# Optimization experiments

Hardware: AMD Instinct MI355X
Metric: run time of the kernel (lower is better)

## Reference

```python
import jax, jax.numpy as jnp
import numpy as np

IN_F, RED, WID, CLS, T = 700, 256, 4096, 20, 100


def _q4(W):
    # per-tensor symmetric INT4 STE: value is quantized, grad is identity
    scale = jnp.maximum(jnp.abs(W).max() / 7.0, 1e-8)
    return W + jax.lax.stop_gradient(jnp.round(W / scale) * scale - W)


def setup_inputs() -> dict:
    key = jax.random.key(0)
    ks = jax.random.split(key, 12)
    B = 64
    x = jax.random.normal(ks[0], (B, T, IN_F), dtype=jnp.float32)
    latent = jax.random.uniform(ks[1], (T,), dtype=jnp.float32)
    spatial_W = jax.random.normal(ks[2], (RED, IN_F), jnp.float32) / np.sqrt(IN_F)
    spatial_b = jnp.zeros((RED,), jnp.float32)
    conv_W = jax.random.normal(ks[3], (RED, RED, 5), jnp.float32) / np.sqrt(RED * 5)
    conv_b = jnp.zeros((RED,), jnp.float32)
    fc1_W = jax.random.normal(ks[4], (WID, RED), jnp.float32) / np.sqrt(RED)
    fc1_b = jnp.zeros((WID,), jnp.float32)
    fc2_W = jax.random.normal(ks[5], (CLS, WID), jnp.float32) / np.sqrt(WID)
    fc2_b = jnp.zeros((CLS,), jnp.float32)
    gain = jnp.asarray(1.0, jnp.float32)
    return {"x": x, "latent": latent, "spatial_W": spatial_W, "spatial_b": spatial_b,
            "conv_W": conv_W, "conv_b": conv_b, "fc1_W": fc1_W, "fc1_b": fc1_b,
            "fc2_W": fc2_W, "fc2_b": fc2_b, "gain": gain}


def _compute_drive(x, latent, spatial_W, spatial_b, conv_W, conv_b, fc1_W, fc1_b, gain):
    # spatial projection (INT4 STE linear) + relu : (B,T,RED)
    xp = jax.nn.relu(jnp.einsum("btf,rf->btr", x, _q4(spatial_W)) + spatial_b)
    # temporal conv1d over T, padding=2 (same), channels RED->RED
    xc = jax.lax.conv_general_dilated(
        xp.transpose(0, 2, 1), conv_W, window_strides=(1,), padding=[(2, 2)],
        dimension_numbers=("NCH", "OIH", "NCH"))
    conv_out = jax.nn.relu(xc + conv_b[None, :, None]).transpose(0, 2, 1)  # (B,T,RED)
    spatial_act = jax.nn.softplus(jnp.einsum("btr,wr->btw", conv_out, _q4(fc1_W)) + fc1_b)
    return spatial_act * latent[None, :, None] * jnp.abs(gain)  # (B,T,WID)


def reference(x, latent, spatial_W, spatial_b, conv_W, conv_b, fc1_W, fc1_b, fc2_W, fc2_b, gain):
    drive = _compute_drive(x, latent, spatial_W, spatial_b, conv_W, conv_b, fc1_W, fc1_b, gain)
    # Poisson spike sampling with straight-through estimator, then clamp at 1
    pois = jax.random.poisson(jax.random.key(42), jax.lax.stop_gradient(drive)).astype(drive.dtype)
    spikes = drive + jax.lax.stop_gradient(pois - drive)
    spikes = jnp.minimum(spikes, 1.0)
    # decay-weighted temporal reduction over T
    decay = jnp.exp(jnp.linspace(-2.0, 0.0, T)).astype(drive.dtype)
    weighted = jnp.einsum("btw,t->bw", spikes, decay)  # (B,WID)
    # dropout in eval mode = identity
    logits = weighted @ _q4(fc2_W).T + fc2_b  # (B,CLS)
    return (logits, spikes, drive)
```

## Files before the change

kernel.cpp:

```cpp
#include <hip/hip_runtime.h>
#include <stdint.h>

#define B 64
#define T 100
#define IN_F 700
#define RED 256
#define WID 4096
#define CLS 20
#define BT (B*T)
#define NELEM (BT*WID)
#define LOGITS_OFF 0
#define SPIKES_OFF (B*CLS)
#define DRIVE_OFF (SPIKES_OFF + NELEM)

#define WS_SLOTS 0
#define WS_W2Q 16
#define WS_XP  (WS_W2Q + CLS*WID)
#define WS_CO  (WS_XP + BT*RED)
#define WS_WEIGHTED (WS_CO + BT*RED)

#define SC_WST 0
#define SC_W1T (SC_WST + IN_F*RED)
#define SC_CWT (SC_W1T + RED*WID)

__host__ __device__ __forceinline__ uint32_t rotl32(uint32_t v, int r) {
  return (v << r) | (v >> (32 - r));
}

__host__ __device__ __forceinline__ void threefry2x32(uint32_t k0, uint32_t k1,
                                                      uint32_t x0, uint32_t x1,
                                                      uint32_t& o0, uint32_t& o1) {
  uint32_t k2 = k0 ^ k1 ^ 0x1BD11BDAu;
  x0 += k0; x1 += k1;
#define TF_R(r) { x0 += x1; x1 = rotl32(x1, (r)); x1 ^= x0; }
  TF_R(13) TF_R(15) TF_R(26) TF_R(6)
  x0 += k1; x1 += k2 + 1u;
  TF_R(17) TF_R(29) TF_R(16) TF_R(24)
  x0 += k2; x1 += k0 + 2u;
  TF_R(13) TF_R(15) TF_R(26) TF_R(6)
  x0 += k0; x1 += k1 + 3u;
  TF_R(17) TF_R(29) TF_R(16) TF_R(24)
  x0 += k1; x1 += k2 + 4u;
  TF_R(13) TF_R(15) TF_R(26) TF_R(6)
  x0 += k2; x1 += k0 + 5u;
#undef TF_R
  o0 = x0; o1 = x1;
}

__global__ void absmax_kernel(const float* __restrict__ w, int n, uint32_t* slot) {
  __shared__ uint32_t sm[256];
  uint32_t m = 0u;
  for (int i = blockIdx.x * 256 + threadIdx.x; i < n; i += gridDim.x * 256)
    m = max(m, __float_as_uint(fabsf(w[i])));
  sm[threadIdx.x] = m;
  __syncthreads();
  for (int s = 128; s > 0; s >>= 1) {
    if (threadIdx.x < s) sm[threadIdx.x] = max(sm[threadIdx.x], sm[threadIdx.x + s]);
    __syncthreads();
  }
  if (threadIdx.x == 0) atomicMax(slot, sm[0]);
}

__global__ void quant_t_kernel(const float* __restrict__ w, float* __restrict__ qT,
                               int Nn, int Kk, const uint32_t* __restrict__ slot) {
  float s = fmaxf(__uint_as_float(*slot) / 7.0f, 1e-8f);
  int id = blockIdx.x * 256 + threadIdx.x;
  if (id < Nn * Kk) {
    int n = id / Kk, k = id - n * Kk;
    qT[(size_t)k * Nn + n] = rintf(w[id] / s) * s;
  }
}

__global__ void quant_kernel(const float* __restrict__ w, float* __restrict__ q,
                             int n, const uint32_t* __restrict__ slot) {
  float s = fmaxf(__uint_as_float(*slot) / 7.0f, 1e-8f);
  int i = blockIdx.x * 256 + threadIdx.x;
  if (i < n) q[i] = rintf(w[i] / s) * s;
}

__global__ void convw_t_kernel(const float* __restrict__ w, float* __restrict__ wt) {
  int id = blockIdx.x * 256 + threadIdx.x;
  if (id < 256 * 1280) {
    int o = id / 1280, r = id - o * 1280;
    int ic = r / 5, h = r - ic * 5;
    wt[(size_t)((h << 8) + ic) * 256 + o] = w[id];
  }
}

template<int SRCA>
__global__ __launch_bounds__(256, 8)
void gemm32_kernel(const float* __restrict__ A, const float* __restrict__ Bt,
                   const float* __restrict__ bias, float* __restrict__ C,
                   int M, int N, int K) {
  constexpr int MT = 32, NT = 64, TM = 2, TN = 4;
  constexpr int ASR = MT + 4, BSR = NT + 4;
  __shared__ float As[32 * ASR];
  __shared__ float Bs[32 * BSR];
  int tid = threadIdx.x;
  int tx = tid & 15, ty = tid >> 4;
  int m0 = blockIdx.x * MT, n0 = blockIdx.y * NT;
  float acc[TM * TN];
#pragma unroll
  for (int i = 0; i < TM * TN; ++i) acc[i] = 0.f;

  for (int kt = 0; kt < K; kt += 32) {
    int klen = K - kt; if (klen > 32) klen = 32;
#pragma unroll
    for (int rep = 0; rep < 4; ++rep) {
      int e = rep * 256 + tid;
      int kk = e & 31, m = e >> 5;
      float v = 0.f;
      if (SRCA == 0) {
        if (kk < klen) v = A[(size_t)(m0 + m) * K + kt + kk];
      } else {
        if (kk < klen) {
          int k = kt + kk;
          int h = k >> 8, ic = k & 255;
          int bt = m0 + m;
          int b = bt / T, t = bt - b * T;
          int tt = t + h - 2;
          if (tt >= 0 && tt < T) v = A[((size_t)(b * T + tt)) * RED + ic];
        }
      }
      As[kk * ASR + m] = v;
    }
#pragma unroll
    for (int rep = 0; rep < 8; ++rep) {
      int e = rep * 256 + tid;
      int kk = e >> 6, n = e & 63;
      float v = 0.f;
      if (kk < klen) v = Bt[(size_t)(kt + kk) * N + n0 + n];
      Bs[kk * BSR + n] = v;
    }
    __syncthreads();
    if (klen == 32) {
#pragma unroll
      for (int kk = 0; kk < 32; ++kk) {
        float a[TM], b[TN];
#pragma unroll
        for (int i = 0; i < TM; ++i) a[i] = As[kk * ASR + ty * TM + i];
#pragma unroll
        for (int d = 0; d < TN; ++d) b[d] = Bs[kk * BSR + tx * TN + d];
#pragma unroll
        for (int j = 0; j < TM; ++j)
#pragma unroll
          for (int d = 0; d < TN; ++d)
            acc[j * TN + d] = fmaf(a[j], b[d], acc[j * TN + d]);
      }
    } else {
      for (int kk = 0; kk < klen; ++kk) {
        float a[TM], b[TN];
#pragma unroll
        for (int i = 0; i < TM; ++i) a[i] = As[kk * ASR + ty * TM + i];
#pragma unroll
        for (int d = 0; d < TN; ++d) b[d] = Bs[kk * BSR + tx * TN + d];
#pragma unroll
        for (int j = 0; j < TM; ++j)
#pragma unroll
          for (int d = 0; d < TN; ++d)
            acc[j * TN + d] = fmaf(a[j], b[d], acc[j * TN + d]);
      }
    }
    __syncthreads();
  }

  float bv[TN];
#pragma unroll
  for (int d = 0; d < TN; ++d) bv[d] = bias[n0 + tx * TN + d];
#pragma unroll
  for (int j = 0; j < TM; ++j) {
    int m = m0 + ty * TM + j;
#pragma unroll
    for (int d = 0; d < TN; ++d)
      C[(size_t)m * N + n0 + tx * TN + d] = fmaxf(acc[j * TN + d] + bv[d], 0.0f);
  }
}

__global__ __launch_bounds__(256, 4)
void fc1_kernel(const float* __restrict__ A, const float* __restrict__ Bt,
                const float* __restrict__ bias, const float* __restrict__ latent,
                const float* __restrict__ gain, float* __restrict__ C,
                int K, int N) {
  constexpr int MT = 128, NT = 128, TM = 8, TN = 8;
  constexpr int ASR = MT + 4, BSR = NT + 4;
  __shared__ float As[32 * ASR];
  __shared__ float Bs[32 * BSR];
  int tid = threadIdx.x;
  int tx = tid & 15, ty = tid >> 4;
  int wid = (blockIdx.x & 7) * 200 + (blockIdx.x >> 3);
  int bx = wid % 50, by = wid / 50;
  int m0 = bx * MT, n0 = by * NT;
  float acc[TM * TN];
#pragma unroll
  for (int i = 0; i < TM * TN; ++i) acc[i] = 0.f;

  for (int kt = 0; kt < K; kt += 32) {
#pragma unroll
    for (int rep = 0; rep < 4; ++rep) {
      int e = rep * 256 + tid;
      int k4 = e & 7, m = e >> 3;
      const float4 v = *(const float4*)&A[(size_t)(m0 + m) * K + kt + k4 * 4];
      As[(k4 * 4 + 0) * ASR + m] = v.x;
      As[(k4 * 4 + 1) * ASR + m] = v.y;
      As[(k4 * 4 + 2) * ASR + m] = v.z;
      As[(k4 * 4 + 3) * ASR + m] = v.w;
    }
#pragma unroll
    for (int rep = 0; rep < 4; ++rep) {
      int e = rep * 256 + tid;
      int n4 = e & 31, kk = e >> 5;
      float4 v = *(const float4*)&Bt[(size_t)(kt + kk) * N + n0 + n4 * 4];
      *(float4*)&Bs[kk * BSR + n4 * 4] = v;
    }
    __syncthreads();
#pragma unroll
    for (int kk = 0; kk < 32; ++kk) {
      float a[TM], b[TN];
#pragma unroll
      for (int i = 0; i < TM; ++i) a[i] = As[kk * ASR + ty * TM + i];
#pragma unroll
      for (int d = 0; d < TN; ++d) b[d] = Bs[kk * BSR + tx * TN + d];
#pragma unroll
      for (int j = 0; j < TM; ++j)
#pragma unroll
        for (int d = 0; d < TN; ++d)
          acc[j * TN + d] = fmaf(a[j], b[d], acc[j * TN + d]);
    }
    __syncthreads();
  }

  float g = fabsf(gain[0]);
  float bv[TN];
#pragma unroll
  for (int d = 0; d < TN; ++d) bv[d] = bias[n0 + tx * TN + d];
#pragma unroll
  for (int j = 0; j < TM; ++j) {
    int bt = m0 + ty * TM + j;
    int q = bt / T;
    float lat = latent[bt - q * T];
    float o[TN];
#pragma unroll
    for (int d = 0; d < TN; ++d) {
      float v = acc[j * TN + d] + bv[d];
      float e = expf(-fabsf(v));
      float l = log1pf(e);
      float sp = fmaxf(v, 0.0f) + l;
      o[d] = (sp * lat) * g;
    }
    float4 o0 = make_float4(o[0], o[1], o[2], o[3]);
    float4 o1 = make_float4(o[4], o[5], o[6], o[7]);
    *(float4*)&C[(size_t)bt * N + n0 + tx * TN + 0] = o0;
    *(float4*)&C[(size_t)bt * N + n0 + tx * TN + 4] = o1;
  }
}

__global__ __launch_bounds__(256) void spike_weighted_kernel(float* __restrict__ out,
                                                             float* __restrict__ wt,
                                                             uint32_t k0, uint32_t k1) {
  __shared__ float dec[128];
  int tid = threadIdx.x;
  if (tid < T) {
    float step = 2.0f / 99.0f;
    float a = step * (float)tid;
    dec[tid] = expf(a - 2.0f);
  }
  __syncthreads();
  int b = blockIdx.x >> 4;
  int w = ((blockIdx.x & 15) << 8) + tid;
  float acc = 0.f;
  for (int t = 0; t < T; ++t) {
    uint32_t p = (uint32_t)((b * T + t) * WID + w);
    float lam = out[DRIVE_OFF + p];
    uint32_t y0, y1;
    threefry2x32(k0, k1, 0u, p, y0, y1);
    uint32_t bits = y0 ^ y1;
    float u = __uint_as_float((bits >> 9) | 0x3f800000u) - 1.0f;
    float s = (lam > 0.0f && logf(u) > -lam) ? 1.0f : 0.0f;
    out[SPIKES_OFF + p] = s;
    acc = fmaf(s, dec[t], acc);
  }
  wt[b * WID + w] = acc;
}

__global__ void logits_kernel(const float* __restrict__ wt,
                              const float* __restrict__ w2,
                              const float* __restrict__ b2,
                              float* __restrict__ out) {
  __shared__ float sm[256];
  int b = blockIdx.x / CLS, c = blockIdx.x - b * CLS;
  const float* wr = wt + (size_t)b * WID;
  const float* w2r = w2 + (size_t)c * WID;
  float p = 0.f;
  for (int w = threadIdx.x; w < WID; w += 256) p = fmaf(wr[w], w2r[w], p);
  sm[threadIdx.x] = p;
  __syncthreads();
  for (int s = 128; s > 0; s >>= 1) {
    if (threadIdx.x < s) sm[threadIdx.x] += sm[threadIdx.x + s];
    __syncthreads();
  }
  if (threadIdx.x == 0) out[LOGITS_OFF + blockIdx.x] = sm[0] + b2[c];
}

extern "C" void kernel_launch(void* const* d_in, const int* in_sizes, int n_in,
                              void* d_out, int out_size, void* d_ws, size_t ws_size,
                              hipStream_t stream) {
  (void)in_sizes; (void)n_in; (void)out_size; (void)ws_size;
  const float* x         = (const float*)d_in[0];
  const float* latent    = (const float*)d_in[1];
  const float* spatial_W = (const float*)d_in[2];
  const float* spatial_b = (const float*)d_in[3];
  const float* conv_W    = (const float*)d_in[4];
  const float* conv_b    = (const float*)d_in[5];
  const float* fc1_W     = (const float*)d_in[6];
  const float* fc1_b     = (const float*)d_in[7];
  const float* fc2_W     = (const float*)d_in[8];
  const float* fc2_b     = (const float*)d_in[9];
  const float* gain      = (const float*)d_in[10];
  float* out = (float*)d_out;
  uint32_t* wsu = (uint32_t*)d_ws;
  float* wsf = (float*)d_ws;
  float* S = out + SPIKES_OFF;

  uint32_t sk0, sk1;
  threefry2x32(0u, 42u, 0u, 1u, sk0, sk1);

  hipMemsetAsync(wsu + WS_SLOTS, 0, 3 * sizeof(uint32_t), stream);
  absmax_kernel<<<64, 256, 0, stream>>>(spatial_W, RED * IN_F, wsu + WS_SLOTS + 0);
  absmax_kernel<<<256, 256, 0, stream>>>(fc1_W, WID * RED, wsu + WS_SLOTS + 1);
  absmax_kernel<<<32, 256, 0, stream>>>(fc2_W, CLS * WID, wsu + WS_SLOTS + 2);

  quant_t_kernel<<<700, 256, 0, stream>>>(spatial_W, S + SC_WST, RED, IN_F, wsu + WS_SLOTS + 0);
  quant_t_kernel<<<4096, 256, 0, stream>>>(fc1_W, S + SC_W1T, WID, RED, wsu + WS_SLOTS + 1);
  quant_kernel<<<320, 256, 0, stream>>>(fc2_W, wsf + WS_W2Q, CLS * WID, wsu + WS_SLOTS + 2);
  convw_t_kernel<<<1280, 256, 0, stream>>>(conv_W, S + SC_CWT);

  gemm32_kernel<0><<<dim3(200, 4), 256, 0, stream>>>(
      x, S + SC_WST, spatial_b, wsf + WS_XP, BT, RED, IN_F);

  gemm32_kernel<1><<<dim3(200, 4), 256, 0, stream>>>(
      wsf + WS_XP, S + SC_CWT, conv_b, wsf + WS_CO, BT, RED, 1280);

  fc1_kernel<<<1600, 256, 0, stream>>>(
      wsf + WS_CO, S + SC_W1T, fc1_b, latent, gain, out + DRIVE_OFF, RED, WID);

  spike_weighted_kernel<<<B * 16, 256, 0, stream>>>(out, wsf + WS_WEIGHTED, sk0, sk1);

  logits_kernel<<<B * CLS, 256, 0, stream>>>(wsf + WS_WEIGHTED, wsf + WS_W2Q, fc2_b, out);
}
```

Measured before the change: 843.1 us.

## Fuse fc1 weight quantization into fc1 GEMM and vectorize gemm32 tile loads

Drops the separate quant_t kernel for fc1_W. The fc1 GEMM now reads the raw row-major weight, quantizes it on the fly using the absmax slot, and writes it transposed into shared memory. The fc1 thread-to-column mapping changes to two 4-wide halves to suit the new Bs layout. The gemm32 A and B tile loads become float4 loads with fewer iterations. The fused path repeats the division and rounding in every block that touches a weight tile, and its transposed shared-memory stores may cause bank conflicts.

After: 734.8 us. 1.15x faster.

```diff
diff --git a/kernel.cpp b/kernel.cpp
--- a/kernel.cpp
+++ b/kernel.cpp
@@ -20,8 +20,7 @@
 #define WS_WEIGHTED (WS_CO + BT*RED)
 
 #define SC_WST 0
-#define SC_W1T (SC_WST + IN_F*RED)
-#define SC_CWT (SC_W1T + RED*WID)
+#define SC_CWT (SC_WST + IN_F*RED)
 
 __host__ __device__ __forceinline__ uint32_t rotl32(uint32_t v, int r) {
   return (v << r) | (v >> (32 - r));
@@ -99,38 +98,40 @@
   int tid = threadIdx.x;
   int tx = tid & 15, ty = tid >> 4;
   int m0 = blockIdx.x * MT, n0 = blockIdx.y * NT;
+  int am = tid >> 3, ak4 = (tid & 7) << 2;
   float acc[TM * TN];
 #pragma unroll
   for (int i = 0; i < TM * TN; ++i) acc[i] = 0.f;
 
   for (int kt = 0; kt < K; kt += 32) {
     int klen = K - kt; if (klen > 32) klen = 32;
-#pragma unroll
-    for (int rep = 0; rep < 4; ++rep) {
-      int e = rep * 256 + tid;
-      int kk = e & 31, m = e >> 5;
-      float v = 0.f;
-      if (SRCA == 0) {
-        if (kk < klen) v = A[(size_t)(m0 + m) * K + kt + kk];
-      } else {
-        if (kk < klen) {
-          int k = kt + kk;
+    {
+      float4 av = make_float4(0.f, 0.f, 0.f, 0.f);
+      if (ak4 < klen) {
+        if (SRCA == 0) {
+          av = *(const float4*)&A[(size_t)(m0 + am) * K + kt + ak4];
+        } else {
+          int k = kt + ak4;
           int h = k >> 8, ic = k & 255;
-          int bt = m0 + m;
+          int bt = m0 + am;
           int b = bt / T, t = bt - b * T;
           int tt = t + h - 2;
-          if (tt >= 0 && tt < T) v = A[((size_t)(b * T + tt)) * RED + ic];
+          if (tt >= 0 && tt < T)
+            av = *(const float4*)&A[((size_t)(b * T + tt)) * RED + ic];
         }
       }
-      As[kk * ASR + m] = v;
-    }
-#pragma unroll
-    for (int rep = 0; rep < 8; ++rep) {
+      As[(ak4 + 0) * ASR + am] = av.x;
+      As[(ak4 + 1) * ASR + am] = av.y;
+      As[(ak4 + 2) * ASR + am] = av.z;
+      As[(ak4 + 3) * ASR + am] = av.w;
+    }
+#pragma unroll
+    for (int rep = 0; rep < 2; ++rep) {
       int e = rep * 256 + tid;
-      int kk = e >> 6, n = e & 63;
-      float v = 0.f;
-      if (kk < klen) v = Bt[(size_t)(kt + kk) * N + n0 + n];
-      Bs[kk * BSR + n] = v;
+      int n4 = (e & 15) << 2, kk = e >> 4;
+      float4 v = make_float4(0.f, 0.f, 0.f, 0.f);
+      if (kk < klen) v = *(const float4*)&Bt[(size_t)(kt + kk) * N + n0 + n4];
+      *(float4*)&Bs[kk * BSR + n4] = v;
     }
     __syncthreads();
     if (klen == 32) {
@@ -177,19 +178,22 @@
 }
 
 __global__ __launch_bounds__(256, 4)
-void fc1_kernel(const float* __restrict__ A, const float* __restrict__ Bt,
+void fc1_kernel(const float* __restrict__ A, const float* __restrict__ W1,
                 const float* __restrict__ bias, const float* __restrict__ latent,
                 const float* __restrict__ gain, float* __restrict__ C,
-                int K, int N) {
+                const uint32_t* __restrict__ slot, int K, int N) {
   constexpr int MT = 128, NT = 128, TM = 8, TN = 8;
   constexpr int ASR = MT + 4, BSR = NT + 4;
   __shared__ float As[32 * ASR];
   __shared__ float Bs[32 * BSR];
+  float qs = fmaxf(__uint_as_float(*slot) / 7.0f, 1e-8f);
   int tid = threadIdx.x;
   int tx = tid & 15, ty = tid >> 4;
   int wid = (blockIdx.x & 7) * 200 + (blockIdx.x >> 3);
   int bx = wid % 50, by = wid / 50;
   int m0 = bx * MT, n0 = by * NT;
+  int bn = tid & 127, kh = (tid >> 7) << 4;
+  const float* wrow = &W1[(size_t)(n0 + bn) * K + kh];
   float acc[TM * TN];
 #pragma unroll
   for (int i = 0; i < TM * TN; ++i) acc[i] = 0.f;
@@ -198,19 +202,21 @@
 #pragma unroll
     for (int rep = 0; rep < 4; ++rep) {
       int e = rep * 256 + tid;
-      int k4 = e & 7, m = e >> 3;
-      const float4 v = *(const float4*)&A[(size_t)(m0 + m) * K + kt + k4 * 4];
-      As[(k4 * 4 + 0) * ASR + m] = v.x;
-      As[(k4 * 4 + 1) * ASR + m] = v.y;
-      As[(k4 * 4 + 2) * ASR + m] = v.z;
-      As[(k4 * 4 + 3) * ASR + m] = v.w;
-    }
-#pragma unroll
-    for (int rep = 0; rep < 4; ++rep) {
-      int e = rep * 256 + tid;
-      int n4 = e & 31, kk = e >> 5;
-      float4 v = *(const float4*)&Bt[(size_t)(kt + kk) * N + n0 + n4 * 4];
-      *(float4*)&Bs[kk * BSR + n4 * 4] = v;
+      int k4 = (e & 7) << 2, m = e >> 3;
+      const float4 v = *(const float4*)&A[(size_t)(m0 + m) * K + kt + k4];
+      As[(k4 + 0) * ASR + m] = v.x;
+      As[(k4 + 1) * ASR + m] = v.y;
+      As[(k4 + 2) * ASR + m] = v.z;
+      As[(k4 + 3) * ASR + m] = v.w;
+    }
+#pragma unroll
+    for (int q4 = 0; q4 < 4; ++q4) {
+      const float4 v = *(const float4*)&wrow[kt + (q4 << 2)];
+      int kk = kh + (q4 << 2);
+      Bs[(kk + 0) * BSR + bn] = rintf(v.x / qs) * qs;
+      Bs[(kk + 1) * BSR + bn] = rintf(v.y / qs) * qs;
+      Bs[(kk + 2) * BSR + bn] = rintf(v.z / qs) * qs;
+      Bs[(kk + 3) * BSR + bn] = rintf(v.w / qs) * qs;
     }
     __syncthreads();
 #pragma unroll
@@ -219,7 +225,9 @@
 #pragma unroll
       for (int i = 0; i < TM; ++i) a[i] = As[kk * ASR + ty * TM + i];
 #pragma unroll
-      for (int d = 0; d < TN; ++d) b[d] = Bs[kk * BSR + tx * TN + d];
+      for (int d = 0; d < 4; ++d) b[d] = Bs[kk * BSR + tx * 4 + d];
+#pragma unroll
+      for (int d = 0; d < 4; ++d) b[4 + d] = Bs[kk * BSR + 64 + tx * 4 + d];
 #pragma unroll
       for (int j = 0; j < TM; ++j)
 #pragma unroll
@@ -232,7 +240,10 @@
   float g = fabsf(gain[0]);
   float bv[TN];
 #pragma unroll
-  for (int d = 0; d < TN; ++d) bv[d] = bias[n0 + tx * TN + d];
+  for (int d = 0; d < 4; ++d) {
+    bv[d] = bias[n0 + tx * 4 + d];
+    bv[4 + d] = bias[n0 + 64 + tx * 4 + d];
+  }
 #pragma unroll
   for (int j = 0; j < TM; ++j) {
     int bt = m0 + ty * TM + j;
@@ -249,8 +260,8 @@
     }
     float4 o0 = make_float4(o[0], o[1], o[2], o[3]);
     float4 o1 = make_float4(o[4], o[5], o[6], o[7]);
-    *(float4*)&C[(size_t)bt * N + n0 + tx * TN + 0] = o0;
-    *(float4*)&C[(size_t)bt * N + n0 + tx * TN + 4] = o1;
+    *(float4*)&C[(size_t)bt * N + n0 + tx * 4] = o0;
+    *(float4*)&C[(size_t)bt * N + n0 + 64 + tx * 4] = o1;
   }
 }
 
@@ -330,7 +341,6 @@
   absmax_kernel<<<32, 256, 0, stream>>>(fc2_W, CLS * WID, wsu + WS_SLOTS + 2);
 
   quant_t_kernel<<<700, 256, 0, stream>>>(spatial_W, S + SC_WST, RED, IN_F, wsu + WS_SLOTS + 0);
-  quant_t_kernel<<<4096, 256, 0, stream>>>(fc1_W, S + SC_W1T, WID, RED, wsu + WS_SLOTS + 1);
   quant_kernel<<<320, 256, 0, stream>>>(fc2_W, wsf + WS_W2Q, CLS * WID, wsu + WS_SLOTS + 2);
   convw_t_kernel<<<1280, 256, 0, stream>>>(conv_W, S + SC_CWT);
 
@@ -341,7 +351,8 @@
       wsf + WS_XP, S + SC_CWT, conv_b, wsf + WS_CO, BT, RED, 1280);
 
   fc1_kernel<<<1600, 256, 0, stream>>>(
-      wsf + WS_CO, S + SC_W1T, fc1_b, latent, gain, out + DRIVE_OFF, RED, WID);
+      wsf + WS_CO, fc1_W, fc1_b, latent, gain, out + DRIVE_OFF,
+      wsu + WS_SLOTS + 1, RED, WID);
 
   spike_weighted_kernel<<<B * 16, 256, 0, stream>>>(out, wsf + WS_WEIGHTED, sk0, sk1);
 
```
